# Optimization experiments

Measured on AMD Instinct MI355X. Metric: run time of the kernel, lower is better.

## Reference

```python
import jax, jax.numpy as jnp
import numpy as np

HIDDEN = 768
NUM_HEADS = 12
HEAD_DIM = HIDDEN // NUM_HEADS
NUM_SELECTED = 64
SCALE = 1.0 / np.sqrt(HEAD_DIM)


def setup_inputs() -> dict:
    key = jax.random.key(0)
    k0, k1, k2, k3, k4 = jax.random.split(key, 5)
    B, S = 1, 2048
    inputs = jax.random.normal(k0, (B, S, HIDDEN), dtype=jnp.float32)
    # nn.Linear weights, stored as [out, in]; applied as x @ W.T
    Wq = jax.random.normal(k1, (HIDDEN, HIDDEN), dtype=jnp.float32) * 0.02
    Wk = jax.random.normal(k2, (HIDDEN, HIDDEN), dtype=jnp.float32) * 0.02
    Wv = jax.random.normal(k3, (HIDDEN, HIDDEN), dtype=jnp.float32) * 0.02
    Wo = jax.random.normal(k4, (HIDDEN, HIDDEN), dtype=jnp.float32) * 0.02
    return {"inputs": inputs, "Wq": Wq, "Wk": Wk, "Wv": Wv, "Wo": Wo}


def reference(inputs, Wq, Wk, Wv, Wo):
    B, S, H = inputs.shape
    K = NUM_SELECTED
    pos = jnp.arange(S)
    window_starts = jnp.clip(pos + 1 - K, 0, None)                      # [S]
    sel = window_starts[:, None] + jnp.arange(K)[None, :]               # [S, K]
    sel = jnp.clip(sel, 0, S - 1)
    causal_mask = sel <= pos[:, None]                                   # [S, K]

    # Per-token linear projections; gathering after the (per-token) linear is
    # mathematically identical to the original gather-then-project.
    q = inputs @ Wq.T                                                   # [B,S,H]
    k_full = inputs @ Wk.T                                              # [B,S,H]
    v_full = inputs @ Wv.T                                              # [B,S,H]

    k = k_full[:, sel]                                                  # [B,S,K,H]
    v = v_full[:, sel]                                                  # [B,S,K,H]

    q = q.reshape(B, S, NUM_HEADS, HEAD_DIM)                            # [B,S,n,d]
    k = k.reshape(B, S, K, NUM_HEADS, HEAD_DIM)                         # [B,S,K,n,d]
    v = v.reshape(B, S, K, NUM_HEADS, HEAD_DIM)

    scores = jnp.einsum("bsnd,bsknd->bnsk", q, k) * SCALE               # [B,n,S,K]
    scores = jnp.where(causal_mask[None, None], scores, -jnp.inf)
    weights = jax.nn.softmax(scores, axis=-1)                           # [B,n,S,K]

    out = jnp.einsum("bnsk,bsknd->bsnd", weights, v)                    # [B,S,n,d]
    out = out.reshape(B, S, H)
    return out @ Wo.T
```

## Files before the change

kernel.cpp:

```cpp
#include <hip/hip_runtime.h>
#include <stdint.h>

#define S_LEN   2048
#define HIDDEN  768
#define NHEADS  12
#define QKV_LD  2304
#define NW      589824

typedef __attribute__((ext_vector_type(8))) short short8;
typedef __attribute__((ext_vector_type(4))) float f32x4;

typedef const __attribute__((address_space(1))) void* gas_ptr;
typedef __attribute__((address_space(3))) void* las_ptr;

__device__ __forceinline__ short f2b(float f) {
    union { float f; uint32_t u; } v; v.f = f;
    uint32_t u = v.u;
    uint32_t r = (u + 0x7FFFu + ((u >> 16) & 1u)) >> 16;
    return (short)r;
}

__global__ __launch_bounds__(256)
void convert_all(const float* __restrict__ X,
                 const float* __restrict__ Wq, const float* __restrict__ Wk,
                 const float* __restrict__ Wv, const float* __restrict__ Wo,
                 short* __restrict__ Xb, short* __restrict__ Wqkvb,
                 short* __restrict__ Wob) {
    int b = blockIdx.x;
    const float* src;
    short* dst;
    int i;
    if (b < 1536) {
        src = X; dst = Xb; i = b * 1024 + threadIdx.x * 4;
    } else {
        int wb = (b - 1536) / 576, lb = (b - 1536) % 576;
        src = wb == 0 ? Wq : wb == 1 ? Wk : wb == 2 ? Wv : Wo;
        dst = wb < 3 ? Wqkvb + wb * NW : Wob;
        i = lb * 1024 + threadIdx.x * 4;
    }
    float4 v = *(const float4*)(src + i);
    *(short4*)(dst + i) = make_short4(f2b(v.x), f2b(v.y), f2b(v.z), f2b(v.w));
}

template<int OUT_BF16>
__device__ __forceinline__ void gemm64x128(const short* __restrict__ A,
    const short* __restrict__ B, void* __restrict__ Cv,
    int bm, int bn, int ldc) {
    __shared__ short sA[2][64 * 64];
    __shared__ short sB[2][128 * 64];

    const int tid = threadIdx.x, lane = tid & 63, w = tid >> 6;
    const int wr = w >> 1, wc = w & 1;

    f32x4 acc[2][4] = {};

    auto stage = [&](int buf, int k0) {
        #pragma unroll
        for (int c = 0; c < 2; ++c) {
            int r = w * 16 + c * 8 + (lane >> 3);
            int scb = ((lane & 7) * 16) ^ ((r & 7) << 4);
            const char* gp = (const char*)(A + (size_t)(bm * 64 + r) * 768 + k0) + scb;
            __builtin_amdgcn_global_load_lds((gas_ptr)gp,
                (las_ptr)((char*)&sA[buf][0] + w * 2048 + c * 1024), 16, 0, 0);
        }
        #pragma unroll
        for (int c = 0; c < 4; ++c) {
            int r = w * 32 + c * 8 + (lane >> 3);
            int scb = ((lane & 7) * 16) ^ ((r & 7) << 4);
            const char* gp = (const char*)(B + (size_t)(bn * 128 + r) * 768 + k0) + scb;
            __builtin_amdgcn_global_load_lds((gas_ptr)gp,
                (las_ptr)((char*)&sB[buf][0] + w * 4096 + c * 1024), 16, 0, 0);
        }
    };

    stage(0, 0);
    __syncthreads();
    int cur = 0;
    for (int t = 0; t < 12; ++t) {
        if (t < 11) stage(cur ^ 1, (t + 1) * 64);
        #pragma unroll
        for (int kh = 0; kh < 2; ++kh) {
            const int kb = kh * 64 + ((lane >> 4) << 4);
            short8 av[2], bv[4];
            #pragma unroll
            for (int mi = 0; mi < 2; ++mi) {
                int row = wr * 32 + mi * 16 + (lane & 15);
                av[mi] = *(const short8*)((const char*)&sA[cur][0] + row * 128 + (kb ^ ((row & 7) << 4)));
            }
            #pragma unroll
            for (int ni = 0; ni < 4; ++ni) {
                int row = wc * 64 + ni * 16 + (lane & 15);
                bv[ni] = *(const short8*)((const char*)&sB[cur][0] + row * 128 + (kb ^ ((row & 7) << 4)));
            }
            #pragma unroll
            for (int mi = 0; mi < 2; ++mi)
                #pragma unroll
                for (int ni = 0; ni < 4; ++ni)
                    acc[mi][ni] = __builtin_amdgcn_mfma_f32_16x16x32_bf16(
                        av[mi], bv[ni], acc[mi][ni], 0, 0, 0);
        }
        __syncthreads();
        cur ^= 1;
    }

    const int crow0 = bm * 64 + wr * 32;
    const int ccol0 = bn * 128 + wc * 64;
    #pragma unroll
    for (int mi = 0; mi < 2; ++mi)
        #pragma unroll
        for (int ni = 0; ni < 4; ++ni)
            #pragma unroll
            for (int r = 0; r < 4; ++r) {
                int grow = crow0 + mi * 16 + ((lane >> 4) << 2) + r;
                int gcol = ccol0 + ni * 16 + (lane & 15);
                if (OUT_BF16)
                    ((short*)Cv)[(size_t)grow * ldc + gcol] = f2b(acc[mi][ni][r]);
                else
                    ((float*)Cv)[(size_t)grow * ldc + gcol] = acc[mi][ni][r];
            }
}

__global__ __launch_bounds__(256)
void gemm_qkv(const short* __restrict__ Xb, const short* __restrict__ Wqkvb,
              short* __restrict__ C) {
    const int bid = blockIdx.x;
    const int sw = (bid & 7) * 72 + (bid >> 3);
    gemm64x128<1>(Xb, Wqkvb, C, sw / 18, sw % 18, QKV_LD);
}

__global__ __launch_bounds__(256)
void gemm_out(const short* __restrict__ A, const short* __restrict__ Wob,
              float* __restrict__ C) {
    const int bid = blockIdx.x;
    const int sw = (bid & 7) * 24 + (bid >> 3);
    gemm64x128<0>(A, Wob, C, sw / 6, sw % 6, HIDDEN);
}

__global__ __launch_bounds__(256)
void attn_mfma(const short* __restrict__ QKV, short* __restrict__ O) {
    __shared__ short sK[128 * 64];
    __shared__ short sVt[64 * 128];
    __shared__ short sP[4][16 * 128];

    const int bid = blockIdx.x;
    const int task = (bid & 7) * 48 + (bid >> 3);
    const int h = task % NHEADS;
    const int s0 = (task / NHEADS) * 64;
    const int tid = threadIdx.x, lane = tid & 63, w = tid >> 6;

    #pragma unroll
    for (int c = 0; c < 4; ++c) {
        int r = (w * 4 + c) * 8 + (lane >> 3);
        int gr = s0 - 64 + r; if (gr < 0) gr = 0;
        int scb = ((lane & 7) * 16) ^ ((r & 7) << 4);
        const char* gp = (const char*)(QKV + (size_t)gr * QKV_LD + 768 + h * 64) + scb;
        __builtin_amdgcn_global_load_lds((gas_ptr)gp,
            (las_ptr)((char*)sK + (w * 4 + c) * 1024), 16, 0, 0);
    }
    {
        const int d0 = (tid & 7) * 8;
        const int kbase = (tid >> 3) * 4;
        short8 v[4];
        #pragma unroll
        for (int i = 0; i < 4; ++i) {
            int gr = s0 - 64 + kbase + i; if (gr < 0) gr = 0;
            v[i] = *(const short8*)(QKV + (size_t)gr * QKV_LD + 1536 + h * 64 + d0);
        }
        #pragma unroll
        for (int j = 0; j < 8; ++j) {
            int row = d0 + j;
            int b = row * 256 + ((kbase * 2) ^ ((row & 7) << 4));
            *(short4*)((char*)sVt + b) = make_short4(v[0][j], v[1][j], v[2][j], v[3][j]);
        }
    }
    const int qrow = w * 16 + (lane & 15);
    short8 qf[2];
    #pragma unroll
    for (int kk = 0; kk < 2; ++kk)
        qf[kk] = *(const short8*)(QKV + (size_t)(s0 + qrow) * QKV_LD + h * 64
                                  + kk * 32 + ((lane >> 4) << 3));
    __syncthreads();

    f32x4 s_acc[8];
    #pragma unroll
    for (int ct = 0; ct < 8; ++ct) {
        s_acc[ct] = (f32x4){0.f, 0.f, 0.f, 0.f};
        int krow = ct * 16 + (lane & 15);
        #pragma unroll
        for (int kk = 0; kk < 2; ++kk) {
            int cb = kk * 64 + ((lane >> 4) << 4);
            short8 kf = *(const short8*)((const char*)sK + krow * 128 + (cb ^ ((krow & 7) << 4)));
            s_acc[ct] = __builtin_amdgcn_mfma_f32_16x16x32_bf16(qf[kk], kf, s_acc[ct], 0, 0, 0);
        }
    }

    const int kcol = lane & 15;
    const int qb = w * 16 + ((lane >> 4) << 2);
    float p[8][4];
    #pragma unroll
    for (int r = 0; r < 4; ++r) {
        int q = qb + r;
        float m = -1e30f;
        #pragma unroll
        for (int ct = 0; ct < 8; ++ct) {
            int kt = ct * 16 + kcol;
            bool valid = (kt > q) && (kt <= q + 64) && (s0 + kt >= 64);
            float sc = valid ? s_acc[ct][r] * 0.125f : -1e30f;
            p[ct][r] = sc;
            m = fmaxf(m, sc);
        }
        #pragma unroll
        for (int off = 1; off < 16; off <<= 1) m = fmaxf(m, __shfl_xor(m, off));
        float sm = 0.f;
        #pragma unroll
        for (int ct = 0; ct < 8; ++ct) {
            float e = __expf(p[ct][r] - m);
            p[ct][r] = e;
            sm += e;
        }
        #pragma unroll
        for (int off = 1; off < 16; off <<= 1) sm += __shfl_xor(sm, off);
        float inv = 1.f / sm;
        #pragma unroll
        for (int ct = 0; ct < 8; ++ct) p[ct][r] *= inv;
    }

    #pragma unroll
    for (int ct = 0; ct < 8; ++ct)
        #pragma unroll
        for (int r = 0; r < 4; ++r) {
            int row = ((lane >> 4) << 2) + r;
            int b = row * 256 + (((ct * 16 + kcol) * 2) ^ ((row & 7) << 4));
            *(short*)((char*)&sP[w][0] + b) = f2b(p[ct][r]);
        }

    short8 pf[4];
    #pragma unroll
    for (int kk = 0; kk < 4; ++kk) {
        int row = lane & 15;
        int cb = kk * 64 + ((lane >> 4) << 4);
        pf[kk] = *(const short8*)((const char*)&sP[w][0] + row * 256 + (cb ^ ((row & 7) << 4)));
    }
    f32x4 o_acc[4];
    #pragma unroll
    for (int nt = 0; nt < 4; ++nt) {
        o_acc[nt] = (f32x4){0.f, 0.f, 0.f, 0.f};
        #pragma unroll
        for (int kk = 0; kk < 4; ++kk) {
            int vrow = nt * 16 + (lane & 15);
            int cb = kk * 64 + ((lane >> 4) << 4);
            short8 vf = *(const short8*)((const char*)sVt + vrow * 256 + (cb ^ ((vrow & 7) << 4)));
            o_acc[nt] = __builtin_amdgcn_mfma_f32_16x16x32_bf16(pf[kk], vf, o_acc[nt], 0, 0, 0);
        }
    }

    #pragma unroll
    for (int nt = 0; nt < 4; ++nt)
        #pragma unroll
        for (int r = 0; r < 4; ++r) {
            int q = s0 + qb + r;
            int dcol = h * 64 + nt * 16 + (lane & 15);
            O[(size_t)q * HIDDEN + dcol] = f2b(o_acc[nt][r]);
        }
}

extern "C" void kernel_launch(void* const* d_in, const int* in_sizes, int n_in,
                              void* d_out, int out_size, void* d_ws, size_t ws_size,
                              hipStream_t stream) {
    const float* X  = (const float*)d_in[0];
    const float* Wq = (const float*)d_in[1];
    const float* Wk = (const float*)d_in[2];
    const float* Wv = (const float*)d_in[3];
    const float* Wo = (const float*)d_in[4];
    float* out = (float*)d_out;

    char* ws = (char*)d_ws;
    short* Xb    = (short*)ws;
    short* Wqkvb = (short*)(ws + 3145728);
    short* Wob   = (short*)(ws + 6684672);
    short* QKVb  = (short*)(ws + 7864320);
    short* Attnb = (short*)(ws + 17301504);

    convert_all<<<1536 + 4 * 576, 256, 0, stream>>>(X, Wq, Wk, Wv, Wo, Xb, Wqkvb, Wob);
    gemm_qkv<<<576, 256, 0, stream>>>(Xb, Wqkvb, QKVb);
    attn_mfma<<<384, 256, 0, stream>>>(QKVb, Attnb);
    gemm_out<<<192, 256, 0, stream>>>(Attnb, Wob, out);
}
```

Measured before the change: 47.65 us.

## Triple-buffer GEMM LDS staging and remap blocks per XCD for locality

The shared 64x128 GEMM goes from double-buffered to triple-buffered LDS staging. Two k-tiles are prefetched ahead, and explicit vmcnt waits plus one barrier per iteration replace the two __syncthreads. The goal is to hide global-to-LDS load latency behind MFMA work and remove one barrier per k-step. Both GEMM kernels also remap block IDs so blocks landing on the same XCD cover a compact 8xN tile region, to improve L2 reuse of A and B. The cost is 1.5x more LDS per block, which could lower occupancy.

Measured after the change: 48.90 us. 1.03x slower.

```diff
diff --git a/kernel.cpp b/kernel.cpp
--- a/kernel.cpp
+++ b/kernel.cpp
@@ -43,11 +43,11 @@
 }
 
 template<int OUT_BF16>
-__device__ __forceinline__ void gemm64x128(const short* __restrict__ A,
+__device__ __forceinline__ void gemm64x128_p2(const short* __restrict__ A,
     const short* __restrict__ B, void* __restrict__ Cv,
     int bm, int bn, int ldc) {
-    __shared__ short sA[2][64 * 64];
-    __shared__ short sB[2][128 * 64];
+    __shared__ short sA[3][64 * 64];
+    __shared__ short sB[3][128 * 64];
 
     const int tid = threadIdx.x, lane = tid & 63, w = tid >> 6;
     const int wr = w >> 1, wc = w & 1;
@@ -74,10 +74,16 @@
     };
 
     stage(0, 0);
-    __syncthreads();
-    int cur = 0;
+    stage(1, 64);
     for (int t = 0; t < 12; ++t) {
-        if (t < 11) stage(cur ^ 1, (t + 1) * 64);
+        if (t < 11) asm volatile("s_waitcnt vmcnt(6)" ::: "memory");
+        else        asm volatile("s_waitcnt vmcnt(0)" ::: "memory");
+        __builtin_amdgcn_s_barrier();
+        asm volatile("" ::: "memory");
+        if (t < 10) stage((t + 2) % 3, (t + 2) * 64);
+
+        const char* bA = (const char*)&sA[t % 3][0];
+        const char* bB = (const char*)&sB[t % 3][0];
         #pragma unroll
         for (int kh = 0; kh < 2; ++kh) {
             const int kb = kh * 64 + ((lane >> 4) << 4);
@@ -85,12 +91,12 @@
             #pragma unroll
             for (int mi = 0; mi < 2; ++mi) {
                 int row = wr * 32 + mi * 16 + (lane & 15);
-                av[mi] = *(const short8*)((const char*)&sA[cur][0] + row * 128 + (kb ^ ((row & 7) << 4)));
+                av[mi] = *(const short8*)(bA + row * 128 + (kb ^ ((row & 7) << 4)));
             }
             #pragma unroll
             for (int ni = 0; ni < 4; ++ni) {
                 int row = wc * 64 + ni * 16 + (lane & 15);
-                bv[ni] = *(const short8*)((const char*)&sB[cur][0] + row * 128 + (kb ^ ((row & 7) << 4)));
+                bv[ni] = *(const short8*)(bB + row * 128 + (kb ^ ((row & 7) << 4)));
             }
             #pragma unroll
             for (int mi = 0; mi < 2; ++mi)
@@ -99,8 +105,7 @@
                     acc[mi][ni] = __builtin_amdgcn_mfma_f32_16x16x32_bf16(
                         av[mi], bv[ni], acc[mi][ni], 0, 0, 0);
         }
-        __syncthreads();
-        cur ^= 1;
+        asm volatile("" ::: "memory");
     }
 
     const int crow0 = bm * 64 + wr * 32;
@@ -123,17 +128,19 @@
 __global__ __launch_bounds__(256)
 void gemm_qkv(const short* __restrict__ Xb, const short* __restrict__ Wqkvb,
               short* __restrict__ C) {
-    const int bid = blockIdx.x;
-    const int sw = (bid & 7) * 72 + (bid >> 3);
-    gemm64x128<1>(Xb, Wqkvb, C, sw / 18, sw % 18, QKV_LD);
+    const int x = blockIdx.x & 7, i = blockIdx.x >> 3;
+    const int bm = (x >> 1) * 8 + i / 9;
+    const int bn = (x & 1) * 9 + i % 9;
+    gemm64x128_p2<1>(Xb, Wqkvb, C, bm, bn, QKV_LD);
 }
 
 __global__ __launch_bounds__(256)
 void gemm_out(const short* __restrict__ A, const short* __restrict__ Wob,
               float* __restrict__ C) {
-    const int bid = blockIdx.x;
-    const int sw = (bid & 7) * 24 + (bid >> 3);
-    gemm64x128<0>(A, Wob, C, sw / 6, sw % 6, HIDDEN);
+    const int x = blockIdx.x & 7, i = blockIdx.x >> 3;
+    const int bm = (x >> 1) * 8 + i / 3;
+    const int bn = (x & 1) * 3 + i % 3;
+    gemm64x128_p2<0>(A, Wob, C, bm, bn, HIDDEN);
 }
 
 __global__ __launch_bounds__(256)
```

## Shrink GEMM tiles to 64x64, remap blocks, and grid-stride conversion kernel

Applied to the files above, without the earlier changes.

The QKV and output GEMMs switch from 64x128 to 64x64 output tiles, which doubles the block count (1152 and 384) so more of the MI355X compute units get work, notably for the small output projection. The block-to-tile mapping is rewritten into an 8-way grouped layout. The fp32-to-bf16 conversion kernel becomes a grid-stride loop over 1024 blocks instead of one block per chunk. Smaller tiles lower per-block operand reuse and add global and LDS traffic per FLOP.

Measured after the change: 49.81 us. +4.5%, slower.

```diff
diff --git a/kernel.cpp b/kernel.cpp
--- a/kernel.cpp
+++ b/kernel.cpp
@@ -26,50 +26,46 @@
                  const float* __restrict__ Wv, const float* __restrict__ Wo,
                  short* __restrict__ Xb, short* __restrict__ Wqkvb,
                  short* __restrict__ Wob) {
-    int b = blockIdx.x;
-    const float* src;
-    short* dst;
-    int i;
-    if (b < 1536) {
-        src = X; dst = Xb; i = b * 1024 + threadIdx.x * 4;
-    } else {
-        int wb = (b - 1536) / 576, lb = (b - 1536) % 576;
-        src = wb == 0 ? Wq : wb == 1 ? Wk : wb == 2 ? Wv : Wo;
-        dst = wb < 3 ? Wqkvb + wb * NW : Wob;
-        i = lb * 1024 + threadIdx.x * 4;
-    }
-    float4 v = *(const float4*)(src + i);
-    *(short4*)(dst + i) = make_short4(f2b(v.x), f2b(v.y), f2b(v.z), f2b(v.w));
+    const int NX4 = 393216, NW4 = 147456, TOT = 983040;
+    for (int idx = blockIdx.x * 256 + threadIdx.x; idx < TOT; idx += 1024 * 256) {
+        const float* src; short* dst; int e;
+        if (idx < NX4) {
+            src = X; dst = Xb; e = idx * 4;
+        } else {
+            int j = idx - NX4;
+            int wb = j / NW4, lb = j % NW4;
+            src = wb == 0 ? Wq : wb == 1 ? Wk : wb == 2 ? Wv : Wo;
+            dst = wb < 3 ? Wqkvb + wb * NW : Wob;
+            e = lb * 4;
+        }
+        float4 v = *(const float4*)(src + e);
+        *(short4*)(dst + e) = make_short4(f2b(v.x), f2b(v.y), f2b(v.z), f2b(v.w));
+    }
 }
 
 template<int OUT_BF16>
-__device__ __forceinline__ void gemm64x128(const short* __restrict__ A,
+__device__ __forceinline__ void gemm64x64(const short* __restrict__ A,
     const short* __restrict__ B, void* __restrict__ Cv,
     int bm, int bn, int ldc) {
     __shared__ short sA[2][64 * 64];
-    __shared__ short sB[2][128 * 64];
+    __shared__ short sB[2][64 * 64];
 
     const int tid = threadIdx.x, lane = tid & 63, w = tid >> 6;
     const int wr = w >> 1, wc = w & 1;
 
-    f32x4 acc[2][4] = {};
+    f32x4 acc[2][2] = {};
 
     auto stage = [&](int buf, int k0) {
         #pragma unroll
         for (int c = 0; c < 2; ++c) {
             int r = w * 16 + c * 8 + (lane >> 3);
             int scb = ((lane & 7) * 16) ^ ((r & 7) << 4);
-            const char* gp = (const char*)(A + (size_t)(bm * 64 + r) * 768 + k0) + scb;
-            __builtin_amdgcn_global_load_lds((gas_ptr)gp,
+            const char* gpA = (const char*)(A + (size_t)(bm * 64 + r) * 768 + k0) + scb;
+            __builtin_amdgcn_global_load_lds((gas_ptr)gpA,
                 (las_ptr)((char*)&sA[buf][0] + w * 2048 + c * 1024), 16, 0, 0);
-        }
-        #pragma unroll
-        for (int c = 0; c < 4; ++c) {
-            int r = w * 32 + c * 8 + (lane >> 3);
-            int scb = ((lane & 7) * 16) ^ ((r & 7) << 4);
-            const char* gp = (const char*)(B + (size_t)(bn * 128 + r) * 768 + k0) + scb;
-            __builtin_amdgcn_global_load_lds((gas_ptr)gp,
-                (las_ptr)((char*)&sB[buf][0] + w * 4096 + c * 1024), 16, 0, 0);
+            const char* gpB = (const char*)(B + (size_t)(bn * 64 + r) * 768 + k0) + scb;
+            __builtin_amdgcn_global_load_lds((gas_ptr)gpB,
+                (las_ptr)((char*)&sB[buf][0] + w * 2048 + c * 1024), 16, 0, 0);
         }
     };
 
@@ -81,21 +77,21 @@
         #pragma unroll
         for (int kh = 0; kh < 2; ++kh) {
             const int kb = kh * 64 + ((lane >> 4) << 4);
-            short8 av[2], bv[4];
+            short8 av[2], bv[2];
             #pragma unroll
             for (int mi = 0; mi < 2; ++mi) {
                 int row = wr * 32 + mi * 16 + (lane & 15);
                 av[mi] = *(const short8*)((const char*)&sA[cur][0] + row * 128 + (kb ^ ((row & 7) << 4)));
             }
             #pragma unroll
-            for (int ni = 0; ni < 4; ++ni) {
-                int row = wc * 64 + ni * 16 + (lane & 15);
+            for (int ni = 0; ni < 2; ++ni) {
+                int row = wc * 32 + ni * 16 + (lane & 15);
                 bv[ni] = *(const short8*)((const char*)&sB[cur][0] + row * 128 + (kb ^ ((row & 7) << 4)));
             }
             #pragma unroll
             for (int mi = 0; mi < 2; ++mi)
                 #pragma unroll
-                for (int ni = 0; ni < 4; ++ni)
+                for (int ni = 0; ni < 2; ++ni)
                     acc[mi][ni] = __builtin_amdgcn_mfma_f32_16x16x32_bf16(
                         av[mi], bv[ni], acc[mi][ni], 0, 0, 0);
         }
@@ -104,11 +100,11 @@
     }
 
     const int crow0 = bm * 64 + wr * 32;
-    const int ccol0 = bn * 128 + wc * 64;
+    const int ccol0 = bn * 64 + wc * 32;
     #pragma unroll
     for (int mi = 0; mi < 2; ++mi)
         #pragma unroll
-        for (int ni = 0; ni < 4; ++ni)
+        for (int ni = 0; ni < 2; ++ni)
             #pragma unroll
             for (int r = 0; r < 4; ++r) {
                 int grow = crow0 + mi * 16 + ((lane >> 4) << 2) + r;
@@ -123,17 +119,19 @@
 __global__ __launch_bounds__(256)
 void gemm_qkv(const short* __restrict__ Xb, const short* __restrict__ Wqkvb,
               short* __restrict__ C) {
-    const int bid = blockIdx.x;
-    const int sw = (bid & 7) * 72 + (bid >> 3);
-    gemm64x128<1>(Xb, Wqkvb, C, sw / 18, sw % 18, QKV_LD);
+    const int x = blockIdx.x & 7, i = blockIdx.x >> 3;
+    const int bm = (x >> 2) * 16 + i / 9;
+    const int bn = (x & 3) * 9 + i % 9;
+    gemm64x64<1>(Xb, Wqkvb, C, bm, bn, QKV_LD);
 }
 
 __global__ __launch_bounds__(256)
 void gemm_out(const short* __restrict__ A, const short* __restrict__ Wob,
               float* __restrict__ C) {
-    const int bid = blockIdx.x;
-    const int sw = (bid & 7) * 24 + (bid >> 3);
-    gemm64x128<0>(A, Wob, C, sw / 6, sw % 6, HIDDEN);
+    const int x = blockIdx.x & 7, i = blockIdx.x >> 3;
+    const int bm = (x >> 2) * 16 + i / 3;
+    const int bn = (x & 3) * 3 + i % 3;
+    gemm64x64<0>(A, Wob, C, bm, bn, HIDDEN);
 }
 
 __global__ __launch_bounds__(256)
@@ -281,8 +279,8 @@
     short* QKVb  = (short*)(ws + 7864320);
     short* Attnb = (short*)(ws + 17301504);
 
-    convert_all<<<1536 + 4 * 576, 256, 0, stream>>>(X, Wq, Wk, Wv, Wo, Xb, Wqkvb, Wob);
-    gemm_qkv<<<576, 256, 0, stream>>>(Xb, Wqkvb, QKVb);
+    convert_all<<<1024, 256, 0, stream>>>(X, Wq, Wk, Wv, Wo, Xb, Wqkvb, Wob);
+    gemm_qkv<<<1152, 256, 0, stream>>>(Xb, Wqkvb, QKVb);
     attn_mfma<<<384, 256, 0, stream>>>(QKVb, Attnb);
-    gemm_out<<<192, 256, 0, stream>>>(Attnb, Wob, out);
-}
+    gemm_out<<<384, 256, 0, stream>>>(Attnb, Wob, out);
+}
```
